# Kernel tuning notes

Measured on AMD Instinct MI355X. Metric: run time of the kernel, lower is better.

## Reference

```python
import jax, jax.numpy as jnp
import numpy as np

V, D, S, B, NL = 32000, 512, 1024, 2, 2
DS, KC, DI, DFF, E, TOPK = 16, 4, 1024, 2048, 8, 2
EPS = 1e-6


def rmsnorm(x, w):
    return x * jax.lax.rsqrt(jnp.mean(x * x, -1, keepdims=True) + EPS) * w


def mamba(x, in_w, conv_w, conv_b, x_proj_w, dt_w, dt_b, A_log, out_w):
    # x: (B, S, D)
    Bb, L, _ = x.shape
    xz = x @ in_w.T                      # (B, S, 2*DI)
    xi, z = jnp.split(xz, 2, axis=-1)    # each (B, S, DI)
    # causal depthwise conv (pad k-1 left == torch pad k-1 both + trim to L)
    xc = jnp.swapaxes(xi, 1, 2)          # (B, DI, S)
    xc = jax.lax.conv_general_dilated(
        xc, conv_w, window_strides=(1,), padding=[(KC - 1, 0)],
        dimension_numbers=("NCH", "OIH", "NCH"), feature_group_count=DI)
    xi = jnp.swapaxes(xc + conv_b[None, :, None], 1, 2)  # (B, S, DI)
    x_dbl = xi @ x_proj_w.T              # (B, S, 2*DS)
    B_param = x_dbl[..., DS:]            # (B, S, DS); first chunk overwritten in source
    delta = jax.nn.softplus(xi @ dt_w.T + dt_b)          # (B, S, DS)
    A = -jnp.exp(A_log)                  # (DI, DS)
    # recurrence coefficients (state dim summed out, as in source)
    a = jnp.exp(delta[:, :, None, :] * A[None, None]).sum(-1)        # (B, S, DI)
    b = xi * (delta * B_param).sum(-1, keepdims=True)                # (B, S, DI)

    def step(y, ab):
        at, bt = ab
        y = at * y + bt
        return y, y

    _, ys = jax.lax.scan(step, jnp.zeros((Bb, DI), x.dtype),
                         (jnp.swapaxes(a, 0, 1), jnp.swapaxes(b, 0, 1)))
    y = jnp.swapaxes(ys, 0, 1)           # (B, S, DI)
    y = y * jax.nn.silu(z)
    return y @ out_w.T                   # (B, S, D)


def moe(x, rw, rb, w1, b1, w2, b2):
    router_logits = x @ rw.T + rb                     # (B, S, E)
    probs = jax.nn.softmax(router_logits, axis=-1)
    topv, topi = jax.lax.top_k(probs, TOPK)
    wts = topv / topv.sum(-1, keepdims=True)          # renormalized gates
    h = jax.nn.gelu(jnp.einsum("bsd,efd->bsef", x, w1) + b1)   # (B, S, E, DFF)
    eo = jnp.einsum("bsef,edf->bsed", h, w2) + b2               # (B, S, E, D)
    sel = jnp.take_along_axis(eo, topi[..., None], axis=2)      # (B, S, K, D)
    out = (wts[..., None] * sel).sum(2)
    # load-balancing aux loss
    f = jax.nn.one_hot(topi, E).sum(2).mean((0, 1)) / TOPK
    P = probs.mean((0, 1))
    aux = E * jnp.sum(f * P)
    return out, aux


def setup_inputs() -> dict:
    key = jax.random.key(0)
    ks = jax.random.split(key, 16)
    f = lambda k, s: jax.random.normal(k, s, dtype=jnp.float32) * 0.02
    return {
        "input_ids": jax.random.randint(ks[0], (B, S), 0, V),
        "tok_emb": f(ks[1], (V, D)),
        "pos_emb": f(ks[2], (S, D)),
        "norm1_w": jnp.ones((NL, D), jnp.float32),
        "norm2_w": jnp.ones((NL, D), jnp.float32),
        "in_proj_w": f(ks[3], (NL, 2 * DI, D)),
        "conv_w": f(ks[4], (NL, DI, 1, KC)),
        "conv_b": jnp.zeros((NL, DI), jnp.float32),
        "x_proj_w": f(ks[5], (NL, 2 * DS, DI)),
        "dt_proj_w": f(ks[6], (NL, DS, DI)),
        "dt_proj_b": jnp.zeros((NL, DS), jnp.float32),
        "A_log": jnp.tile(jnp.log(jnp.arange(1, DS + 1, dtype=jnp.float32)), (NL, DI, 1)),
        "D_param": jnp.ones((NL, DI), jnp.float32),  # unused in forward, as in source
        "out_proj_w": f(ks[7], (NL, D, DI)),
        "router_w": f(ks[8], (NL, E, D)),
        "router_b": jnp.zeros((NL, E), jnp.float32),
        "w1": f(ks[9], (NL, E, DFF, D)),
        "b1": jnp.zeros((NL, E, DFF), jnp.float32),
        "w2": f(ks[10], (NL, E, D, DFF)),
        "b2": jnp.zeros((NL, E, D), jnp.float32),
        "final_norm_w": jnp.ones((D,), jnp.float32),
        "lm_head_w": f(ks[11], (V, D)),
    }


def reference(input_ids, tok_emb, pos_emb, norm1_w, norm2_w, in_proj_w, conv_w,
              conv_b, x_proj_w, dt_proj_w, dt_proj_b, A_log, D_param, out_proj_w,
              router_w, router_b, w1, b1, w2, b2, final_norm_w, lm_head_w):
    x = tok_emb[input_ids] + pos_emb[None, :, :]
    aux_total = jnp.zeros((), x.dtype)
    for l in range(NL):
        m = mamba(rmsnorm(x, norm1_w[l]), in_proj_w[l], conv_w[l], conv_b[l],
                  x_proj_w[l], dt_proj_w[l], dt_proj_b[l], A_log[l], out_proj_w[l])
        x = x + m
        ff, aux = moe(rmsnorm(x, norm2_w[l]), router_w[l], router_b[l],
                      w1[l], b1[l], w2[l], b2[l])
        x = x + ff
        aux_total = aux_total + aux
    x = rmsnorm(x, final_norm_w)
    logits = x @ lm_head_w.T
    return logits, aux_total
```

## Files before the change

### kernel.cpp

```cpp
#include <hip/hip_runtime.h>
#include <math.h>

#define S_    1024
#define D_    512
#define DI_   1024
#define DS_   16
#define KC_   4
#define E_    8
#define DFF_  2048
#define NTOK  2048
#define VOCAB 32000
#define NCHUNK 16
#define CHL    64
#define NSLOT 4096

typedef unsigned short ushort;
typedef unsigned int   uint;
typedef __attribute__((ext_vector_type(8))) short short8;
typedef __attribute__((ext_vector_type(4))) float f32x4;

#define IN_US   0ull
#define INL_US  1048576ull
#define OUT_US  2097152ull
#define OUTL_US 2621440ull
#define W1_US   3145728ull
#define W1L_US  11534336ull
#define W2_US   19922944ull
#define W2L_US  28311552ull
#define LAYER_US 36700160ull
#define LM_US   73400320ull
#define IN4   262144
#define OUT4  393216
#define W14   2490368
#define L4    4587520
#define LM4   4096000
#define LMEND 13271040
#define TOT4  13279232

__device__ __forceinline__ float gelu_sig(float x){
  float u = x*(1.5957691216057308f + 0.07135481627f*x*x);
  return x / (1.0f + expf(-u));
}
__device__ __forceinline__ ushort f2bf_rnd(float f){
  uint u = __float_as_uint(f);
  return (ushort)((u + 0x8000u) >> 16);
}
__device__ __forceinline__ float bf2f(ushort h){
  return __uint_as_float(((uint)h) << 16);
}
__device__ __forceinline__ void split1(float f, ushort& h, ushort& l){
  h = f2bf_rnd(f);
  float fh = bf2f(h);
  l = (ushort)(__float_as_uint(f - fh) >> 16);
}

__global__ __launch_bounds__(128) void k_embed(const int* __restrict__ ids,
    const float* __restrict__ tok, const float* __restrict__ pos, float* __restrict__ x){
  int t  = blockIdx.x;
  int d4 = threadIdx.x << 2;
  int s  = t & (S_-1);
  int id = ids[t];
  float4 tv = *(const float4*)(tok + (size_t)id*D_ + d4);
  float4 pv = *(const float4*)(pos + (size_t)s*D_ + d4);
  float4 o; o.x=tv.x+pv.x; o.y=tv.y+pv.y; o.z=tv.z+pv.z; o.w=tv.w+pv.w;
  *(float4*)(x + (size_t)t*D_ + d4) = o;
}

__global__ __launch_bounds__(256) void k_split_all(
    const float* __restrict__ in_w, const float* __restrict__ out_w,
    const float* __restrict__ w1, const float* __restrict__ w2,
    const float* __restrict__ lm, const float* __restrict__ Alog,
    ushort* __restrict__ wsp, float* __restrict__ negA){
  int g = blockIdx.x*256 + threadIdx.x;
  if (g >= TOT4) return;
  if (g < 2*L4){
    int l = (g < L4) ? 0 : 1;
    int r = g - l*L4;
    const float* src; size_t dh_off, dl_off;
    if (r < IN4){
      src = in_w + (size_t)l*1048576 + (size_t)r*4;
      dh_off = (size_t)l*LAYER_US + IN_US  + (size_t)r*4;
      dl_off = (size_t)l*LAYER_US + INL_US + (size_t)r*4;
    } else if (r < OUT4){
      int r2 = r - IN4;
      src = out_w + (size_t)l*524288 + (size_t)r2*4;
      dh_off = (size_t)l*LAYER_US + OUT_US  + (size_t)r2*4;
      dl_off = (size_t)l*LAYER_US + OUTL_US + (size_t)r2*4;
    } else if (r < W14){
      int r3 = r - OUT4;
      src = w1 + (size_t)l*8388608 + (size_t)r3*4;
      dh_off = (size_t)l*LAYER_US + W1_US  + (size_t)r3*4;
      dl_off = (size_t)l*LAYER_US + W1L_US + (size_t)r3*4;
    } else {
      int r4 = r - W14;
      src = w2 + (size_t)l*8388608 + (size_t)r4*4;
      dh_off = (size_t)l*LAYER_US + W2_US  + (size_t)r4*4;
      dl_off = (size_t)l*LAYER_US + W2L_US + (size_t)r4*4;
    }
    float4 v = *(const float4*)src;
    ushort h0,h1,h2,h3,l0,l1,l2,l3;
    split1(v.x,h0,l0); split1(v.y,h1,l1); split1(v.z,h2,l2); split1(v.w,h3,l3);
    *(uint2*)(wsp + dh_off) = make_uint2((uint)h0|((uint)h1<<16), (uint)h2|((uint)h3<<16));
    *(uint2*)(wsp + dl_off) = make_uint2((uint)l0|((uint)l1<<16), (uint)l2|((uint)l3<<16));
  } else if (g < LMEND){
    int r = g - 2*L4;
    float4 v = *(const float4*)(lm + (size_t)r*4);
    ushort h0 = f2bf_rnd(v.x), h1 = f2bf_rnd(v.y), h2 = f2bf_rnd(v.z), h3 = f2bf_rnd(v.w);
    *(uint2*)(wsp + LM_US + (size_t)r*4) = make_uint2((uint)h0|((uint)h1<<16), (uint)h2|((uint)h3<<16));
  } else {
    int r = g - LMEND;
    float4 v = *(const float4*)(Alog + (size_t)r*4);
    float4 o; o.x=-expf(v.x); o.y=-expf(v.y); o.z=-expf(v.z); o.w=-expf(v.w);
    *(float4*)(negA + (size_t)r*4) = o;
  }
}

template<int ADD>
__global__ __launch_bounds__(128) void k_rmsnorm_split(float* __restrict__ x,
    const float* __restrict__ P3, const int* __restrict__ slotmap,
    const float* __restrict__ w, ushort* __restrict__ oh, ushort* __restrict__ ol){
  int t = blockIdx.x;
  int d4 = threadIdx.x << 2;
  float4 v = *(const float4*)(x + (size_t)t*D_ + d4);
  if (ADD){
    int s0 = slotmap[2*t], s1 = slotmap[2*t+1];
    #pragma unroll
    for (int ks=0; ks<4; ++ks){
      float4 p0 = *(const float4*)(P3 + ((size_t)ks*NSLOT + s0)*D_ + d4);
      float4 p1 = *(const float4*)(P3 + ((size_t)ks*NSLOT + s1)*D_ + d4);
      v.x += p0.x + p1.x; v.y += p0.y + p1.y; v.z += p0.z + p1.z; v.w += p0.w + p1.w;
    }
    *(float4*)(x + (size_t)t*D_ + d4) = v;
  }
  float ss = v.x*v.x + v.y*v.y + v.z*v.z + v.w*v.w;
  #pragma unroll
  for (int off=32; off>=1; off>>=1) ss += __shfl_down(ss, off);
  __shared__ float sred[2];
  if ((threadIdx.x & 63) == 0) sred[threadIdx.x >> 6] = ss;
  __syncthreads();
  float total = sred[0] + sred[1];
  float scale = 1.0f / sqrtf(total * (1.0f/D_) + 1e-6f);
  float4 wv = *(const float4*)(w + d4);
  float4 o; o.x=v.x*scale*wv.x; o.y=v.y*scale*wv.y; o.z=v.z*scale*wv.z; o.w=v.w*scale*wv.w;
  ushort h0,h1,h2,h3,l0,l1,l2,l3;
  split1(o.x,h0,l0); split1(o.y,h1,l1); split1(o.z,h2,l2); split1(o.w,h3,l3);
  *(uint2*)(oh + (size_t)t*D_ + d4) = make_uint2((uint)h0|((uint)h1<<16), (uint)h2|((uint)h3<<16));
  *(uint2*)(ol + (size_t)t*D_ + d4) = make_uint2((uint)l0|((uint)l1<<16), (uint)l2|((uint)l3<<16));
}

__global__ __launch_bounds__(128) void k_rmsnorm_router(float* __restrict__ x,
    const float* __restrict__ P2, const float* __restrict__ w,
    const float* __restrict__ rw, const float* __restrict__ rb,
    ushort* __restrict__ oh, ushort* __restrict__ ol,
    float* __restrict__ probs, float* __restrict__ topw, int* __restrict__ topi){
  int t = blockIdx.x;
  int tid = threadIdx.x;
  int d4 = tid << 2;
  float4 v = *(const float4*)(x + (size_t)t*D_ + d4);
  #pragma unroll
  for (int ks=0; ks<4; ++ks){
    float4 p = *(const float4*)(P2 + (size_t)ks*NTOK*D_ + (size_t)t*D_ + d4);
    v.x += p.x; v.y += p.y; v.z += p.z; v.w += p.w;
  }
  *(float4*)(x + (size_t)t*D_ + d4) = v;
  float ss = v.x*v.x + v.y*v.y + v.z*v.z + v.w*v.w;
  #pragma unroll
  for (int off=32; off>=1; off>>=1) ss += __shfl_down(ss, off);
  __shared__ float sred[2];
  __shared__ float lg2[2][E_];
  __shared__ float lg[E_];
  if ((tid & 63) == 0) sred[tid >> 6] = ss;
  __syncthreads();
  float total = sred[0] + sred[1];
  float scale = 1.0f / sqrtf(total * (1.0f/D_) + 1e-6f);
  float4 wv = *(const float4*)(w + d4);
  float4 o; o.x=v.x*scale*wv.x; o.y=v.y*scale*wv.y; o.z=v.z*scale*wv.z; o.w=v.w*scale*wv.w;
  ushort h0,h1,h2,h3,l0,l1,l2,l3;
  split1(o.x,h0,l0); split1(o.y,h1,l1); split1(o.z,h2,l2); split1(o.w,h3,l3);
  *(uint2*)(oh + (size_t)t*D_ + d4) = make_uint2((uint)h0|((uint)h1<<16), (uint)h2|((uint)h3<<16));
  *(uint2*)(ol + (size_t)t*D_ + d4) = make_uint2((uint)l0|((uint)l1<<16), (uint)l2|((uint)l3<<16));
  int lane = tid & 63, wid2 = tid >> 6;
  #pragma unroll
  for (int e=0;e<E_;e++){
    const float* rr = rw + (size_t)e*D_ + d4;
    float p = o.x*rr[0] + o.y*rr[1] + o.z*rr[2] + o.w*rr[3];
    #pragma unroll
    for (int off=32; off>=1; off>>=1) p += __shfl_down(p, off);
    if (lane==0) lg2[wid2][e] = p;
  }
  __syncthreads();
  if (tid==0){
    #pragma unroll
    for (int e=0;e<E_;e++) lg[e] = lg2[0][e] + lg2[1][e] + rb[e];
    float mx = lg[0];
    #pragma unroll
    for (int e=1;e<E_;e++) mx = fmaxf(mx, lg[e]);
    float pe[E_]; float sum = 0.f;
    #pragma unroll
    for (int e=0;e<E_;e++){ pe[e] = expf(lg[e]-mx); sum += pe[e]; }
    #pragma unroll
    for (int e=0;e<E_;e++){ pe[e] /= sum; probs[(size_t)t*E_ + e] = pe[e]; }
    int i1 = 0;
    #pragma unroll
    for (int e=1;e<E_;e++) if (pe[e] > pe[i1]) i1 = e;
    int i2 = (i1==0) ? 1 : 0;
    #pragma unroll
    for (int e=0;e<E_;e++) if (e!=i1 && pe[e] > pe[i2]) i2 = e;
    float wsum = pe[i1] + pe[i2];
    topw[t*2]   = pe[i1]/wsum;
    topw[t*2+1] = pe[i2]/wsum;
    topi[t*2] = i1; topi[t*2+1] = i2;
  }
}

template<int EPI, int NT, int KSP>
__global__ __launch_bounds__(256, 2) void gemm_mfma(
    const ushort* __restrict__ Ah, const ushort* __restrict__ Al,
    const ushort* __restrict__ Whb, const ushort* __restrict__ Wlb,
    float* __restrict__ Cb, ushort* __restrict__ Chh, ushort* __restrict__ Chl,
    const float* __restrict__ biasb, const float* __restrict__ slotw,
    const int* __restrict__ gidx, const int* __restrict__ offs,
    int M, int N, int K)
{
  int e, ks;
  if (KSP > 1){ e = blockIdx.z / KSP; ks = blockIdx.z % KSP; }
  else        { e = blockIdx.z;       ks = 0; }
  int off = 0, cnt = M;
  if (EPI==1 || EPI==3){
    off = offs[e];
    cnt = offs[e+1] - off;
    if ((int)(blockIdx.x*128) >= cnt) return;
  }
  const size_t wbase = (size_t)((EPI==1||EPI==3) ? e : 0) * N * K;
  const ushort* Wh = Whb + wbase;
  const ushort* Wl = Wlb + wbase;
  const float* bias = (EPI==1||EPI==3) ? (biasb + (size_t)e * N) : biasb;

  __shared__ ushort As_h[128][40];
  __shared__ ushort Ws_h[128][40];
  __shared__ ushort As_l[(NT>1)?128:1][40];
  __shared__ ushort Ws_l[(NT>1)?128:1][40];

  const int tid  = threadIdx.x;
  const int row0 = blockIdx.x * 128;
  const int col0 = blockIdx.y * 128;
  const int sr = tid >> 1;
  const int sh = (tid & 1) << 4;

  int aidx;
  if (EPI==1){ int lrr = row0 + sr; if (lrr > cnt-1) lrr = cnt-1; aidx = gidx[off + lrr]; }
  else if (EPI==3){ int lrr = row0 + sr; if (lrr > cnt-1) lrr = cnt-1; aidx = off + lrr; }
  else aidx = row0 + sr;
  const ushort* arh = Ah + (size_t)aidx*K;
  const ushort* arl = Al + (size_t)aidx*K;
  const ushort* wrh = Wh + (size_t)(col0 + sr)*K;
  const ushort* wrl = Wl + (size_t)(col0 + sr)*K;

  const int lane = tid & 63;
  const int wid  = tid >> 6;
  const int wrM  = (wid >> 1) * 64;
  const int wcN  = (wid & 1) * 64;
  const int lr   = lane & 15;
  const int kq   = lane >> 4;

  f32x4 zero = {0.f, 0.f, 0.f, 0.f};
  f32x4 acc[4][4];
  #pragma unroll
  for (int i=0;i<4;i++)
    #pragma unroll
    for (int j=0;j<4;j++) acc[i][j] = zero;

  const int k0 = ks * (K / KSP);
  const int k1 = k0 + (K / KSP);

  short8 rah[2], ral[2], rwh[2], rwl[2];
  rah[0]=*(const short8*)(arh+k0+sh); rah[1]=*(const short8*)(arh+k0+sh+8);
  rwh[0]=*(const short8*)(wrh+k0+sh); rwh[1]=*(const short8*)(wrh+k0+sh+8);
  if (NT>1){
    ral[0]=*(const short8*)(arl+k0+sh); ral[1]=*(const short8*)(arl+k0+sh+8);
    rwl[0]=*(const short8*)(wrl+k0+sh); rwl[1]=*(const short8*)(wrl+k0+sh+8);
  }

  for (int kk=k0; kk<k1; kk+=32){
    __syncthreads();
    *(short8*)&As_h[sr][sh]   = rah[0];  *(short8*)&As_h[sr][sh+8] = rah[1];
    *(short8*)&Ws_h[sr][sh]   = rwh[0];  *(short8*)&Ws_h[sr][sh+8] = rwh[1];
    if (NT>1){
      *(short8*)&As_l[sr][sh]   = ral[0];  *(short8*)&As_l[sr][sh+8] = ral[1];
      *(short8*)&Ws_l[sr][sh]   = rwl[0];  *(short8*)&Ws_l[sr][sh+8] = rwl[1];
    }
    if (kk + 32 < k1){
      int kn = kk + 32 + sh;
      rah[0]=*(const short8*)(arh+kn); rah[1]=*(const short8*)(arh+kn+8);
      rwh[0]=*(const short8*)(wrh+kn); rwh[1]=*(const short8*)(wrh+kn+8);
      if (NT>1){
        ral[0]=*(const short8*)(arl+kn); ral[1]=*(const short8*)(arl+kn+8);
        rwl[0]=*(const short8*)(wrl+kn); rwl[1]=*(const short8*)(wrl+kn+8);
      }
    }
    __syncthreads();

    short8 fah[4], fal[4], fbh[4], fbl[4];
    #pragma unroll
    for (int f=0; f<4; ++f){
      int rA = wrM + f*16 + lr;
      fah[f] = *(const short8*)&As_h[rA][kq*8];
      int rB = wcN + f*16 + lr;
      fbh[f] = *(const short8*)&Ws_h[rB][kq*8];
      if (NT>1){
        fal[f] = *(const short8*)&As_l[rA][kq*8];
        fbl[f] = *(const short8*)&Ws_l[rB][kq*8];
      }
    }
    #pragma unroll
    for (int i=0;i<4;i++)
      #pragma unroll
      for (int j=0;j<4;j++){
        f32x4 c = acc[i][j];
        if (NT==4) c = __builtin_amdgcn_mfma_f32_16x16x32_bf16(fal[i], fbl[j], c, 0,0,0);
        if (NT>1){
          c = __builtin_amdgcn_mfma_f32_16x16x32_bf16(fal[i], fbh[j], c, 0,0,0);
          c = __builtin_amdgcn_mfma_f32_16x16x32_bf16(fah[i], fbl[j], c, 0,0,0);
        }
        c = __builtin_amdgcn_mfma_f32_16x16x32_bf16(fah[i], fbh[j], c, 0,0,0);
        acc[i][j] = c;
      }
  }

  float bj[4];
  if (EPI==1 || EPI==3){
    #pragma unroll
    for (int j=0;j<4;j++) bj[j] = bias[col0 + wcN + j*16 + lr];
  }
  #pragma unroll
  for (int i=0;i<4;i++){
    #pragma unroll
    for (int jj=0;jj<4;jj++){
      int rt   = wrM + i*16 + kq*4 + jj;
      int grow = row0 + rt;
      if (EPI==0){
        float* cr = Cb + (size_t)grow*N + col0 + wcN + lr;
        #pragma unroll
        for (int j=0;j<4;j++) cr[j*16] = acc[i][j][jj];
      } else if (EPI==2){
        float* cr = Cb + (size_t)ks*M*N + (size_t)grow*N + col0 + wcN + lr;
        #pragma unroll
        for (int j=0;j<4;j++) cr[j*16] = acc[i][j][jj];
      } else if (EPI==1){
        if (grow < cnt){
          int slot = off + grow;
          size_t base = (size_t)slot*N + col0 + wcN + lr;
          #pragma unroll
          for (int j=0;j<4;j++){
            float g = gelu_sig(acc[i][j][jj] + bj[j]);
            ushort hh, ll; split1(g, hh, ll);
            Chh[base + j*16] = hh; Chl[base + j*16] = ll;
          }
        }
      } else {
        if (grow < cnt){
          int slot = off + grow;
          float sw = slotw[slot];
          float* cr = Cb + ((size_t)ks*NSLOT + slot)*N + col0 + wcN + lr;
          #pragma unroll
          for (int j=0;j<4;j++){
            float v = acc[i][j][jj];
            if (ks==0) v += bj[j];
            cr[j*16] = sw*v;
          }
        }
      }
    }
  }
}

__global__ __launch_bounds__(256) void k_convab(const float* __restrict__ xz,
    const float* __restrict__ cw, const float* __restrict__ cb,
    const float* __restrict__ xpw, const float* __restrict__ dtw,
    const float* __restrict__ dtb, const float* __restrict__ negA,
    float* __restrict__ a, float* __restrict__ bb){
  int t = blockIdx.x;
  int b = t >> 10, s = t & (S_-1);
  int tid = threadIdx.x;
  int c0 = tid << 2;
  __shared__ float xrow[DI_];
  __shared__ float outv[32];
  __shared__ float dl[DS_+1];
  float4 acc = *(const float4*)(cb + c0);
  #pragma unroll
  for (int k=0;k<KC_;k++){
    int ss = s - (KC_-1) + k;
    if (ss >= 0){
      float4 xv = *(const float4*)(xz + ((size_t)(b*S_+ss))*(2*DI_) + c0);
      acc.x += xv.x * cw[(c0+0)*KC_ + k];
      acc.y += xv.y * cw[(c0+1)*KC_ + k];
      acc.z += xv.z * cw[(c0+2)*KC_ + k];
      acc.w += xv.w * cw[(c0+3)*KC_ + k];
    }
  }
  *(float4*)(xrow + c0) = acc;
  __syncthreads();
  int wid = tid >> 6, lane = tid & 63;
  #pragma unroll
  for (int oi=0; oi<8; ++oi){
    int o = wid*8 + oi;
    const float* wr = (o < 16) ? (xpw + (size_t)(DS_ + o)*DI_) : (dtw + (size_t)(o-16)*DI_);
    float sum = 0.f;
    #pragma unroll
    for (int j=0;j<16;j++) sum += xrow[lane + 64*j] * wr[lane + 64*j];
    #pragma unroll
    for (int off=32; off>=1; off>>=1) sum += __shfl_down(sum, off);
    if (lane == 0) outv[o] = sum;
  }
  __syncthreads();
  if (tid < DS_){
    float d  = outv[16+tid] + dtb[tid];
    float sp = fmaxf(d, 0.f) + log1pf(expf(-fabsf(d)));
    dl[tid] = sp;
    float pr = sp * outv[tid];
    #pragma unroll
    for (int off=8; off>=1; off>>=1) pr += __shfl_down(pr, off);
    if (tid == 0) dl[DS_] = pr;
  }
  __syncthreads();
  float sdbv = dl[DS_];
  float av[4];
  #pragma unroll
  for (int i=0;i<4;i++){
    const float* nA = negA + (size_t)(c0+i)*DS_;
    float sum = 0.f;
    #pragma unroll
    for (int ds=0; ds<DS_; ds++) sum += expf(dl[ds] * nA[ds]);
    av[i] = sum;
  }
  *(float4*)(a + (size_t)t*DI_ + c0) = make_float4(av[0],av[1],av[2],av[3]);
  float4 bv; bv.x=acc.x*sdbv; bv.y=acc.y*sdbv; bv.z=acc.z*sdbv; bv.w=acc.w*sdbv;
  *(float4*)(bb + (size_t)t*DI_ + c0) = bv;
}

__global__ __launch_bounds__(256) void k_scan1(const float* __restrict__ a,
    const float* __restrict__ bb, float* __restrict__ aprod, float* __restrict__ yend){
  int g  = blockIdx.x*256 + threadIdx.x;
  int di = g & (DI_-1);
  int c  = (g >> 10) & (NCHUNK-1);
  int b  = g >> 14;
  float ap = 1.f, y = 0.f;
  size_t base = ((size_t)b*S_ + (size_t)c*CHL)*DI_ + di;
  #pragma unroll 4
  for (int i=0;i<CHL;i++){
    float at = a[base + (size_t)i*DI_], bt = bb[base + (size_t)i*DI_];
    y = at*y + bt; ap *= at;
  }
  aprod[g] = ap; yend[g] = y;
}

__global__ __launch_bounds__(256) void k_scan2(const float* __restrict__ a,
    const float* __restrict__ bb, const float* __restrict__ xz,
    const float* __restrict__ aprod, const float* __restrict__ yend,
    ushort* __restrict__ yh, ushort* __restrict__ yl){
  int g  = blockIdx.x*256 + threadIdx.x;
  int di = g & (DI_-1);
  int c  = (g >> 10) & (NCHUNK-1);
  int b  = g >> 14;
  float y = 0.f;
  for (int j=0;j<c;j++){
    int gg = ((b*NCHUNK + j) << 10) + di;
    y = aprod[gg]*y + yend[gg];
  }
  size_t base = ((size_t)b*S_ + (size_t)c*CHL)*DI_ + di;
  #pragma unroll 4
  for (int i=0;i<CHL;i++){
    float at = a[base + (size_t)i*DI_], bt = bb[base + (size_t)i*DI_];
    y = at*y + bt;
    float z = xz[((size_t)(b*S_ + c*CHL + i))*(2*DI_) + DI_ + di];
    float sil = z / (1.f + expf(-z));
    float v = y * sil;
    ushort hh, ll; split1(v, hh, ll);
    yh[base + (size_t)i*DI_] = hh;
    yl[base + (size_t)i*DI_] = ll;
  }
}

__global__ __launch_bounds__(512) void k_compact_aux(const int* __restrict__ topi,
    const float* __restrict__ topw, const float* __restrict__ probs,
    int* __restrict__ gidx, float* __restrict__ asgw, int* __restrict__ slotmap,
    int* __restrict__ offs, float* __restrict__ dst, int first){
  int tid = threadIdx.x;
  int e = tid >> 6, lane = tid & 63;
  __shared__ unsigned char stop[NTOK*2];
  __shared__ float stw[NTOK*2];
  __shared__ int counts[E_];
  __shared__ float red[8][E_];
  for (int i = tid; i < NTOK*2; i += 512){
    stop[i] = (unsigned char)topi[i];
    stw[i]  = topw[i];
  }
  float ps[E_];
  #pragma unroll
  for (int q=0;q<E_;q++) ps[q]=0.f;
  for (int t = tid; t < NTOK; t += 512){
    float4 p0 = *(const float4*)(probs + (size_t)t*E_);
    float4 p1 = *(const float4*)(probs + (size_t)t*E_ + 4);
    ps[0]+=p0.x; ps[1]+=p0.y; ps[2]+=p0.z; ps[3]+=p0.w;
    ps[4]+=p1.x; ps[5]+=p1.y; ps[6]+=p1.z; ps[7]+=p1.w;
  }
  #pragma unroll
  for (int q=0;q<E_;q++){
    float v = ps[q];
    #pragma unroll
    for (int off=32; off>=1; off>>=1) v += __shfl_down(v, off);
    if (lane==0) red[e][q] = v;
  }
  __syncthreads();
  int cnt = 0;
  for (int c=0; c<NTOK/64; ++c){
    int t = c*64 + lane;
    bool flag = (stop[2*t]==e) || (stop[2*t+1]==e);
    unsigned long long m = __ballot(flag);
    cnt += __popcll(m);
  }
  if (lane==0) counts[e] = cnt;
  __syncthreads();
  int base = 0;
  for (int i=0;i<e;i++) base += counts[i];
  if (lane==0) offs[e] = base;
  if (tid==0){
    int tot=0;
    for (int i=0;i<E_;i++) tot += counts[i];
    offs[E_] = tot;
  }
  int run = base;
  for (int c=0; c<NTOK/64; ++c){
    int t = c*64 + lane;
    int which = (stop[2*t]==e) ? 0 : ((stop[2*t+1]==e) ? 1 : -1);
    bool flag = which >= 0;
    unsigned long long m = __ballot(flag);
    int rank = __popcll(m & ((1ull<<lane)-1ull));
    if (flag){
      int pos = run + rank;
      gidx[pos] = t;
      asgw[pos] = stw[2*t+which];
      slotmap[2*t+which] = pos;
    }
    run += __popcll(m);
  }
  if (tid==0){
    float aux = 0.f;
    #pragma unroll
    for (int i=0;i<E_;i++){
      float P = 0.f;
      #pragma unroll
      for (int wdd=0; wdd<8; ++wdd) P += red[wdd][i];
      P *= (1.0f/NTOK);
      float f = (float)counts[i] * (1.0f/(NTOK*2.0f));
      aux += f*P;
    }
    aux *= (float)E_;
    if (first) dst[0] = aux; else dst[0] += aux;
  }
}

extern "C" void kernel_launch(void* const* d_in, const int* in_sizes, int n_in,
                              void* d_out, int out_size, void* d_ws, size_t ws_size,
                              hipStream_t stream) {
  const int*   input_ids  = (const int*)  d_in[0];
  const float* tok_emb    = (const float*)d_in[1];
  const float* pos_emb    = (const float*)d_in[2];
  const float* norm1_w    = (const float*)d_in[3];
  const float* norm2_w    = (const float*)d_in[4];
  const float* in_proj_w  = (const float*)d_in[5];
  const float* conv_w     = (const float*)d_in[6];
  const float* conv_b     = (const float*)d_in[7];
  const float* x_proj_w   = (const float*)d_in[8];
  const float* dt_proj_w  = (const float*)d_in[9];
  const float* dt_proj_b  = (const float*)d_in[10];
  const float* A_log      = (const float*)d_in[11];
  const float* out_proj_w = (const float*)d_in[13];
  const float* router_w   = (const float*)d_in[14];
  const float* router_b   = (const float*)d_in[15];
  const float* w1         = (const float*)d_in[16];
  const float* b1         = (const float*)d_in[17];
  const float* w2         = (const float*)d_in[18];
  const float* b2         = (const float*)d_in[19];
  const float* final_norm = (const float*)d_in[20];
  const float* lm_head_w  = (const float*)d_in[21];
  float* out = (float*)d_out;

  float* f0 = (float*)d_ws;
  float*  x    = f0;
  ushort* xnh  = (ushort*)(f0 + 1048576);
  ushort* xnl  = xnh + 1048576;
  float*  xz   = f0 + 2097152;
  float*  a    = f0 + 6291456;
  float*  bb   = f0 + 8388608;
  ushort* yh   = (ushort*)(f0 + 10485760);
  ushort* yl   = yh + 2097152;
  ushort* hh   = (ushort*)(f0 + 12582912);
  ushort* hl   = hh + 8388608;
  float*  P2   = f0 + 20971520;
  float*  P3   = f0 + 25165824;
  ushort* wsplit = (ushort*)(f0 + 33554432);
  float*  negA = f0 + 78446592;
  float*  aprod= negA + 32768;
  float*  yendb= aprod + 32768;
  float*  probs= yendb + 32768;
  float*  topw = probs + 16384;
  float*  asgw = topw + 4096;
  int*    topi = (int*)(asgw + 4096);
  int*    gidx = topi + 4096;
  int*    slotmap = gidx + 4096;
  int*    offs = slotmap + 4096;

  float* aux_dst = out + (size_t)NTOK*VOCAB;

  k_split_all<<<(TOT4+255)/256, 256, 0, stream>>>(in_proj_w, out_proj_w, w1, w2,
                                                  lm_head_w, A_log, wsplit, negA);
  k_embed<<<NTOK, 128, 0, stream>>>(input_ids, tok_emb, pos_emb, x);

  for (int l=0; l<2; ++l){
    ushort* L = wsplit + (size_t)l*LAYER_US;
    if (l == 0)
      k_rmsnorm_split<0><<<NTOK, 128, 0, stream>>>(x, nullptr, nullptr,
          norm1_w + (size_t)l*D_, xnh, xnl);
    else
      k_rmsnorm_split<1><<<NTOK, 128, 0, stream>>>(x, P3, slotmap,
          norm1_w + (size_t)l*D_, xnh, xnl);
    gemm_mfma<0,3,1><<<dim3(16,16,1), 256, 0, stream>>>(xnh, xnl, L+IN_US, L+INL_US,
        xz, nullptr, nullptr, nullptr, nullptr, nullptr, nullptr, NTOK, 2*DI_, D_);
    k_convab<<<NTOK, 256, 0, stream>>>(xz, conv_w + (size_t)l*DI_*KC_, conv_b + (size_t)l*DI_,
                                       x_proj_w + (size_t)l*2*DS_*DI_,
                                       dt_proj_w + (size_t)l*DS_*DI_, dt_proj_b + (size_t)l*DS_,
                                       negA + (size_t)l*DI_*DS_, a, bb);
    k_scan1<<<(NTOK*NCHUNK)/256, 256, 0, stream>>>(a, bb, aprod, yendb);
    k_scan2<<<(NTOK*NCHUNK)/256, 256, 0, stream>>>(a, bb, xz, aprod, yendb, yh, yl);
    gemm_mfma<2,3,4><<<dim3(16,4,4), 256, 0, stream>>>(yh, yl, L+OUT_US, L+OUTL_US,
        P2, nullptr, nullptr, nullptr, nullptr, nullptr, nullptr, NTOK, D_, DI_);
    k_rmsnorm_router<<<NTOK, 128, 0, stream>>>(x, P2, norm2_w + (size_t)l*D_,
        router_w + (size_t)l*E_*D_, router_b + (size_t)l*E_,
        xnh, xnl, probs, topw, topi);
    k_compact_aux<<<1, 512, 0, stream>>>(topi, topw, probs, gidx, asgw, slotmap, offs,
                                         aux_dst, l==0 ? 1 : 0);
    gemm_mfma<1,3,1><<<dim3(16,16,8), 256, 0, stream>>>(xnh, xnl, L+W1_US, L+W1L_US,
        nullptr, hh, hl, b1 + (size_t)l*E_*DFF_, nullptr, gidx, offs, 0, DFF_, D_);
    gemm_mfma<3,3,4><<<dim3(16,4,32), 256, 0, stream>>>(hh, hl, L+W2_US, L+W2L_US,
        P3, nullptr, nullptr, b2 + (size_t)l*E_*D_, asgw, gidx, offs, 0, D_, DFF_);
  }

  k_rmsnorm_split<1><<<NTOK, 128, 0, stream>>>(x, P3, slotmap, final_norm, xnh, xnl);
  gemm_mfma<0,1,1><<<dim3(16,250,1), 256, 0, stream>>>(xnh, nullptr, wsplit + LM_US, nullptr,
      out, nullptr, nullptr, nullptr, nullptr, nullptr, nullptr, NTOK, VOCAB, D_);
}
```

Baseline: 965.6 us.

## Load GEMM tiles directly to LDS with XOR-swizzled layout

Replaces the register-staged global→LDS tile copy in the MFMA GEMM with global_load_lds direct-to-LDS transfers, using an unpadded 32-wide LDS layout with XOR swizzle to avoid bank conflicts on fragment reads. Raises the occupancy hint from 2 to 4 blocks per SM. This frees VGPRs and removes the copy through registers, but it drops the register prefetch of the next K tile, so load latency is no longer overlapped with MFMA work except through higher occupancy.

```diff
diff --git a/kernel.cpp b/kernel.cpp
--- a/kernel.cpp
+++ b/kernel.cpp
@@ -52,6 +52,11 @@
   h = f2bf_rnd(f);
   float fh = bf2f(h);
   l = (ushort)(__float_as_uint(f - fh) >> 16);
+}
+__device__ __forceinline__ void gl16(void* lds, const void* g){
+  __builtin_amdgcn_global_load_lds(
+      (const __attribute__((address_space(1))) void*)g,
+      (__attribute__((address_space(3))) void*)lds, 16, 0, 0);
 }
 
 __global__ __launch_bounds__(128) void k_embed(const int* __restrict__ ids,
@@ -214,17 +219,17 @@
 }
 
 template<int EPI, int NT, int KSP>
-__global__ __launch_bounds__(256, 2) void gemm_mfma(
-    const ushort* __restrict__ Ah, const ushort* __restrict__ Al,
+__global__ __launch_bounds__(256, 4) void gemm_mfma(
+    const ushort* __restrict__ Ahg, const ushort* __restrict__ Alg,
     const ushort* __restrict__ Whb, const ushort* __restrict__ Wlb,
     float* __restrict__ Cb, ushort* __restrict__ Chh, ushort* __restrict__ Chl,
     const float* __restrict__ biasb, const float* __restrict__ slotw,
     const int* __restrict__ gidx, const int* __restrict__ offs,
     int M, int N, int K)
 {
-  int e, ks;
-  if (KSP > 1){ e = blockIdx.z / KSP; ks = blockIdx.z % KSP; }
-  else        { e = blockIdx.z;       ks = 0; }
+  int e, ksp;
+  if (KSP > 1){ e = blockIdx.z / KSP; ksp = blockIdx.z % KSP; }
+  else        { e = blockIdx.z;       ksp = 0; }
   int off = 0, cnt = M;
   if (EPI==1 || EPI==3){
     off = offs[e];
@@ -232,36 +237,60 @@
     if ((int)(blockIdx.x*128) >= cnt) return;
   }
   const size_t wbase = (size_t)((EPI==1||EPI==3) ? e : 0) * N * K;
-  const ushort* Wh = Whb + wbase;
-  const ushort* Wl = Wlb + wbase;
+  const ushort* Whg = Whb + wbase;
+  const ushort* Wlg = Wlb + wbase;
   const float* bias = (EPI==1||EPI==3) ? (biasb + (size_t)e * N) : biasb;
 
-  __shared__ ushort As_h[128][40];
-  __shared__ ushort Ws_h[128][40];
-  __shared__ ushort As_l[(NT>1)?128:1][40];
-  __shared__ ushort Ws_l[(NT>1)?128:1][40];
+  __shared__ ushort sAh[128*32];
+  __shared__ ushort sWh[128*32];
+  __shared__ ushort sAl[(NT>1)?(128*32):8];
+  __shared__ ushort sWl[(NT>1)?(128*32):8];
 
   const int tid  = threadIdx.x;
   const int row0 = blockIdx.x * 128;
   const int col0 = blockIdx.y * 128;
-  const int sr = tid >> 1;
-  const int sh = (tid & 1) << 4;
-
-  int aidx;
-  if (EPI==1){ int lrr = row0 + sr; if (lrr > cnt-1) lrr = cnt-1; aidx = gidx[off + lrr]; }
-  else if (EPI==3){ int lrr = row0 + sr; if (lrr > cnt-1) lrr = cnt-1; aidx = off + lrr; }
-  else aidx = row0 + sr;
-  const ushort* arh = Ah + (size_t)aidx*K;
-  const ushort* arl = Al + (size_t)aidx*K;
-  const ushort* wrh = Wh + (size_t)(col0 + sr)*K;
-  const ushort* wrl = Wl + (size_t)(col0 + sr)*K;
-
   const int lane = tid & 63;
   const int wid  = tid >> 6;
-  const int wrM  = (wid >> 1) * 64;
-  const int wcN  = (wid & 1) * 64;
-  const int lr   = lane & 15;
-  const int kq   = lane >> 4;
+
+  const int srow0  = wid*32 + (lane>>2);
+  const int srow1  = srow0 + 16;
+  const int schunk = (lane&3) ^ ((lane>>2)&3);
+  const int ldsb0  = (wid*32)      * 32;
+  const int ldsb1  = (wid*32 + 16) * 32;
+
+  const int k0 = ksp * (K / KSP);
+  const int nk = K / KSP;
+
+  int ar0, ar1;
+  if (EPI==1){
+    int l0i = row0 + srow0; if (l0i > cnt-1) l0i = cnt-1;
+    int l1i = row0 + srow1; if (l1i > cnt-1) l1i = cnt-1;
+    ar0 = gidx[off + l0i]; ar1 = gidx[off + l1i];
+  } else if (EPI==3){
+    int l0i = row0 + srow0; if (l0i > cnt-1) l0i = cnt-1;
+    int l1i = row0 + srow1; if (l1i > cnt-1) l1i = cnt-1;
+    ar0 = off + l0i; ar1 = off + l1i;
+  } else {
+    ar0 = row0 + srow0; ar1 = row0 + srow1;
+  }
+  const ushort* gah0 = Ahg + (size_t)ar0*K + k0 + schunk*8;
+  const ushort* gah1 = Ahg + (size_t)ar1*K + k0 + schunk*8;
+  const ushort* gwh0 = Whg + (size_t)(col0 + srow0)*K + k0 + schunk*8;
+  const ushort* gwh1 = Whg + (size_t)(col0 + srow1)*K + k0 + schunk*8;
+  const ushort* gal0 = nullptr; const ushort* gal1 = nullptr;
+  const ushort* gwl0 = nullptr; const ushort* gwl1 = nullptr;
+  if (NT>1){
+    gal0 = Alg + (size_t)ar0*K + k0 + schunk*8;
+    gal1 = Alg + (size_t)ar1*K + k0 + schunk*8;
+    gwl0 = Wlg + (size_t)(col0 + srow0)*K + k0 + schunk*8;
+    gwl1 = Wlg + (size_t)(col0 + srow1)*K + k0 + schunk*8;
+  }
+
+  const int lr  = lane & 15;
+  const int kq  = lane >> 4;
+  const int kx  = ((kq ^ (lr & 3)) << 3);
+  const int wrM = (wid >> 1) * 64;
+  const int wcN = (wid & 1) * 64;
 
   f32x4 zero = {0.f, 0.f, 0.f, 0.f};
   f32x4 acc[4][4];
@@ -270,33 +299,17 @@
     #pragma unroll
     for (int j=0;j<4;j++) acc[i][j] = zero;
 
-  const int k0 = ks * (K / KSP);
-  const int k1 = k0 + (K / KSP);
-
-  short8 rah[2], ral[2], rwh[2], rwl[2];
-  rah[0]=*(const short8*)(arh+k0+sh); rah[1]=*(const short8*)(arh+k0+sh+8);
-  rwh[0]=*(const short8*)(wrh+k0+sh); rwh[1]=*(const short8*)(wrh+k0+sh+8);
-  if (NT>1){
-    ral[0]=*(const short8*)(arl+k0+sh); ral[1]=*(const short8*)(arl+k0+sh+8);
-    rwl[0]=*(const short8*)(wrl+k0+sh); rwl[1]=*(const short8*)(wrl+k0+sh+8);
-  }
-
-  for (int kk=k0; kk<k1; kk+=32){
+  for (int kk=0; kk<nk; kk+=32){
     __syncthreads();
-    *(short8*)&As_h[sr][sh]   = rah[0];  *(short8*)&As_h[sr][sh+8] = rah[1];
-    *(short8*)&Ws_h[sr][sh]   = rwh[0];  *(short8*)&Ws_h[sr][sh+8] = rwh[1];
+    gl16(&sAh[ldsb0], gah0 + kk);
+    gl16(&sAh[ldsb1], gah1 + kk);
+    gl16(&sWh[ldsb0], gwh0 + kk);
+    gl16(&sWh[ldsb1], gwh1 + kk);
     if (NT>1){
-      *(short8*)&As_l[sr][sh]   = ral[0];  *(short8*)&As_l[sr][sh+8] = ral[1];
-      *(short8*)&Ws_l[sr][sh]   = rwl[0];  *(short8*)&Ws_l[sr][sh+8] = rwl[1];
-    }
-    if (kk + 32 < k1){
-      int kn = kk + 32 + sh;
-      rah[0]=*(const short8*)(arh+kn); rah[1]=*(const short8*)(arh+kn+8);
-      rwh[0]=*(const short8*)(wrh+kn); rwh[1]=*(const short8*)(wrh+kn+8);
-      if (NT>1){
-        ral[0]=*(const short8*)(arl+kn); ral[1]=*(const short8*)(arl+kn+8);
-        rwl[0]=*(const short8*)(wrl+kn); rwl[1]=*(const short8*)(wrl+kn+8);
-      }
+      gl16(&sAl[ldsb0], gal0 + kk);
+      gl16(&sAl[ldsb1], gal1 + kk);
+      gl16(&sWl[ldsb0], gwl0 + kk);
+      gl16(&sWl[ldsb1], gwl1 + kk);
     }
     __syncthreads();
 
@@ -304,12 +317,12 @@
     #pragma unroll
     for (int f=0; f<4; ++f){
       int rA = wrM + f*16 + lr;
-      fah[f] = *(const short8*)&As_h[rA][kq*8];
       int rB = wcN + f*16 + lr;
-      fbh[f] = *(const short8*)&Ws_h[rB][kq*8];
+      fah[f] = *(const short8*)&sAh[rA*32 + kx];
+      fbh[f] = *(const short8*)&sWh[rB*32 + kx];
       if (NT>1){
-        fal[f] = *(const short8*)&As_l[rA][kq*8];
-        fbl[f] = *(const short8*)&Ws_l[rB][kq*8];
+        fal[f] = *(const short8*)&sAl[rA*32 + kx];
+        fbl[f] = *(const short8*)&sWl[rB*32 + kx];
       }
     }
     #pragma unroll
@@ -343,7 +356,7 @@
         #pragma unroll
         for (int j=0;j<4;j++) cr[j*16] = acc[i][j][jj];
       } else if (EPI==2){
-        float* cr = Cb + (size_t)ks*M*N + (size_t)grow*N + col0 + wcN + lr;
+        float* cr = Cb + (size_t)ksp*M*N + (size_t)grow*N + col0 + wcN + lr;
         #pragma unroll
         for (int j=0;j<4;j++) cr[j*16] = acc[i][j][jj];
       } else if (EPI==1){
@@ -361,11 +374,11 @@
         if (grow < cnt){
           int slot = off + grow;
           float sw = slotw[slot];
-          float* cr = Cb + ((size_t)ks*NSLOT + slot)*N + col0 + wcN + lr;
+          float* cr = Cb + ((size_t)ksp*NSLOT + slot)*N + col0 + wcN + lr;
           #pragma unroll
           for (int j=0;j<4;j++){
             float v = acc[i][j][jj];
-            if (ks==0) v += bj[j];
+            if (ksp==0) v += bj[j];
             cr[j*16] = sw*v;
           }
         }
```

Measured after the change: 932.1 us. 3.5% less time.
